# Optimization experiments

Hardware: AMD Instinct MI355X
Metric: run time of the kernel (lower is better)

## Reference

```python
import jax, jax.numpy as jnp
import numpy as np

HIDDEN = 768
NUM_BLOCKS = 8
BLOCK = HIDDEN // NUM_BLOCKS
BASE_THR, K_DECAY, MIN_THR = 0.01, 20.0, 0.0005


def _threshold(height, width):
    # wavenumber-dependent soft-shrink threshold T(k), shape [H, W//2+1]
    fu = jnp.fft.fftfreq(height, d=1.0).astype(jnp.float32)[:, None]
    fv = jnp.fft.rfftfreq(width, d=1.0).astype(jnp.float32)[None, :]
    k = jnp.sqrt(fu ** 2 + fv ** 2) * max(height, width)
    thr = BASE_THR * jnp.exp(-0.5 * (k / K_DECAY) ** 2)
    return jnp.maximum(thr, MIN_THR)


def setup_inputs() -> dict:
    key = jax.random.key(0)
    kx, k1, k2, k3, k4 = jax.random.split(key, 5)
    scale = 0.02
    x = jax.random.normal(kx, (4, 128, 128, HIDDEN), dtype=jnp.float32)
    w1 = scale * jax.random.normal(k1, (2, NUM_BLOCKS, BLOCK, BLOCK), dtype=jnp.float32)
    b1 = scale * jax.random.normal(k2, (2, NUM_BLOCKS, BLOCK), dtype=jnp.float32)
    w2 = scale * jax.random.normal(k3, (2, NUM_BLOCKS, BLOCK, BLOCK), dtype=jnp.float32)
    b2 = scale * jax.random.normal(k4, (2, NUM_BLOCKS, BLOCK), dtype=jnp.float32)
    return {"x": x, "w1": w1, "b1": b1, "w2": w2, "b2": b2}


def reference(x, w1, b1, w2, b2):
    dtype = x.dtype
    bias = x
    xf = x.astype(jnp.float32)
    B, H, W, C = xf.shape
    Wc = W // 2 + 1
    # rfft2 over spatial dims, orthonormal
    Xc = jnp.fft.rfft2(xf, axes=(1, 2), norm='ortho')
    Xc = Xc.reshape(B, H, Wc, NUM_BLOCKS, BLOCK)
    xr, xi = jnp.real(Xc), jnp.imag(Xc)
    mm = lambda t, w: jnp.einsum('bhwni,nio->bhwno', t, w)
    # complex block-diagonal 2-layer MLP
    o1r = jax.nn.relu(mm(xr, w1[0]) - mm(xi, w1[1]) + b1[0])
    o1i = jax.nn.relu(mm(xi, w1[0]) + mm(xr, w1[1]) + b1[1])
    o2r = mm(o1r, w2[0]) - mm(o1i, w2[1]) + b2[0]
    o2i = mm(o1i, w2[0]) + mm(o1r, w2[1]) + b2[1]
    # soft-shrink on complex magnitude with wavenumber-dependent threshold
    mag = jnp.sqrt(o2r ** 2 + o2i ** 2 + 1e-8)
    thr = _threshold(H, W)[None, :, :, None, None]  # [1,H,Wc,1,1]
    sf = jax.nn.relu(mag - thr) / mag
    Yc = (o2r * sf) + 1j * (o2i * sf)
    Yc = Yc.reshape(B, H, Wc, C)
    y = jnp.fft.irfft2(Yc, s=(H, W), axes=(1, 2), norm='ortho')
    return y.astype(dtype) + bias
```

## Files before the change

kernel.cpp:

```cpp
#include <hip/hip_runtime.h>
#include <hip/hip_bf16.h>
#include <math.h>


#define HD   768
#define NBLK 8
#define HH   128
#define WW   128
#define WC   65
#define NPOS (HH * WC)

constexpr float SC    = 0.08838834764831845f;
constexpr float TWOPI = 6.28318530717958647692f;

constexpr int TM_OFF     = 0;
constexpr int TW_OFF     = 49152;
constexpr int TWI_OFF    = 69632;
constexpr int WF_OFF     = 90112;
constexpr int WF_END_U16 = 679936;
constexpr size_t A_UINTS = (size_t)4 * NPOS * HD;

typedef __attribute__((ext_vector_type(8))) short short8;
typedef __attribute__((ext_vector_type(4))) float f32x4;

#define MFMA __builtin_amdgcn_mfma_f32_16x16x32_bf16

static __device__ inline unsigned short f2bf(float f) {
  __hip_bfloat16 h = __float2bfloat16(f);
  return __builtin_bit_cast(unsigned short, h);
}
static __device__ inline unsigned int pack2(float re, float im) {
  return (unsigned int)f2bf(re) | ((unsigned int)f2bf(im) << 16);
}
static __device__ inline float lo2f(unsigned int u) {
  return __builtin_bit_cast(float, u << 16);
}
static __device__ inline float hi2f(unsigned int u) {
  return __builtin_bit_cast(float, u & 0xffff0000u);
}

__global__ __launch_bounds__(256) void k_prep(const float* __restrict__ w1,
                                              const float* __restrict__ b1,
                                              const float* __restrict__ w2,
                                              const float* __restrict__ b2,
                                              unsigned short* __restrict__ wf,
                                              float* __restrict__ bpk) {
  const int blk = blockIdx.x, t = threadIdx.x;
  if (blk < 16) {
    const int layer = blk >> 3, n = blk & 7;
    const float* w  = layer ? w2 : w1;
    const float* bs = layer ? b2 : b1;
    unsigned short* dst = wf + WF_OFF + (size_t)blk * (72 * 512);
    for (int e = t; e < 72 * 512; e += 256) {
      int f = e >> 9, idx = e & 511;
      int kk = f / 12, nt = f - kk * 12;
      int lane = idx >> 3, j = idx & 7;
      int k  = kk * 32 + (lane >> 4) * 8 + j;
      int cc = nt * 16 + (lane & 15);
      float v;
      if (k < 96) v = (cc < 96) ? w[(size_t)n * 9216 + k * 96 + cc]
                                : w[(size_t)(8 + n) * 9216 + k * 96 + (cc - 96)];
      else        v = (cc < 96) ? -w[(size_t)(8 + n) * 9216 + (k - 96) * 96 + cc]
                                :  w[(size_t)n * 9216 + (k - 96) * 96 + (cc - 96)];
      dst[e] = f2bf(v);
    }
    for (int c = t; c < 192; c += 256)
      bpk[blk * 192 + c] = (c < 96) ? bs[n * 96 + c] : bs[(8 + n) * 96 + (c - 96)];
  } else if (blk == 16) {
    for (int e = t; e < 96 * 512; e += 256) {
      int f = e >> 9, idx = e & 511;
      int part = f >> 5, rem = f & 31, kot = rem >> 2, kk = rem & 3;
      int lane = idx >> 3, j = idx & 7;
      int ko = kot * 16 + (lane & 15);
      int r  = kk * 32 + (lane >> 4) * 8 + j;
      float sn, cs; sincosf((TWOPI / 128.f) * (float)((ko * r) & 127), &sn, &cs);
      float v = (part == 0) ? cs : (part == 1) ? sn : -sn;
      wf[TM_OFF + (size_t)f * 512 + idx] = f2bf(v * SC);
    }
  } else if (blk == 17) {
    for (int e = t; e < 40 * 512; e += 256) {
      int f = e >> 9, idx = e & 511;
      int mt = f >> 2, kk = f & 3;
      int lane = idx >> 3, j = idx & 7;
      int row = mt * 16 + (lane & 15);
      int r   = kk * 32 + (lane >> 4) * 8 + j;
      int kor = (row < 80) ? row : row - 80;
      float sn, cs; sincosf((TWOPI / 128.f) * (float)((kor * r) & 127), &sn, &cs);
      wf[TW_OFF + (size_t)f * 512 + idx] = f2bf((row < 80 ? cs : -sn) * SC);
    }
  } else {
    for (int e = t; e < 40 * 512; e += 256) {
      int f = e >> 9, idx = e & 511;
      int mt = f / 5, kk = f - mt * 5;
      int lane = idx >> 3, j = idx & 7;
      int wr = mt * 16 + (lane & 15);
      int k  = kk * 32 + (lane >> 4) * 8 + j;
      float v = 0.f;
      if (k < 80) {
        int kb = k;
        if (kb <= 64) {
          float sn, cs; sincosf((TWOPI / 128.f) * (float)((wr * kb) & 127), &sn, &cs);
          v = SC * ((kb == 0 || kb == 64) ? 1.f : 2.f) * cs;
        }
      } else {
        int kb = k - 80;
        if (kb >= 1 && kb <= 63) {
          float sn, cs; sincosf((TWOPI / 128.f) * (float)((wr * kb) & 127), &sn, &cs);
          v = -2.f * SC * sn;
        }
      }
      wf[TWI_OFF + (size_t)f * 512 + idx] = f2bf(v);
    }
  }
}

__global__ __launch_bounds__(256) void k_fft_w(const float* __restrict__ x,
                                               unsigned int* __restrict__ A,
                                               const unsigned short* __restrict__ wf) {
  __shared__ unsigned short Xt[64 * 136];
  const int h = blockIdx.x, c0 = blockIdx.y * 64, b = blockIdx.z, t = threadIdx.x;
  const int wv = t >> 6, lane = t & 63, l15 = lane & 15, lg = lane >> 4;
  const float* xp = x + ((size_t)(b * HH + h)) * WW * HD + c0;
  for (int idx = t; idx < 128 * 64; idx += 256) {
    int r = idx >> 6, ch = idx & 63;
    Xt[ch * 136 + r] = f2bf(xp[(size_t)r * HD + ch]);
  }
  __syncthreads();
  const unsigned short* tw = wf + TW_OFF;
  f32x4 acc[10];
#pragma unroll
  for (int m = 0; m < 10; ++m) acc[m] = { 0.f, 0.f, 0.f, 0.f };
#pragma unroll
  for (int kk = 0; kk < 4; ++kk) {
    short8 bq = *(const short8*)&Xt[(wv * 16 + l15) * 136 + kk * 32 + lg * 8];
#pragma unroll
    for (int m = 0; m < 10; ++m) {
      short8 a = *(const short8*)&tw[(size_t)(m * 4 + kk) * 512 + lane * 8];
      acc[m] = MFMA(a, bq, acc[m], 0, 0, 0);
    }
  }
  unsigned int* Ao = A + ((size_t)b * NPOS + h * WC) * HD + c0 + wv * 16 + l15;
#pragma unroll
  for (int q = 0; q < 5; ++q)
#pragma unroll
    for (int r = 0; r < 4; ++r) {
      int ko = q * 16 + lg * 4 + r;
      if (ko <= 64) Ao[(size_t)ko * HD] = pack2(acc[q][r], acc[5 + q][r]);
    }
}

__global__ __launch_bounds__(256) void k_ifft_w(const unsigned int* __restrict__ A,
                                                const unsigned int* __restrict__ Bp,
                                                float* __restrict__ out,
                                                const unsigned short* __restrict__ wf) {
  __shared__ unsigned short Zt[64 * 168];
  const int h = blockIdx.x, c0 = blockIdx.y * 64, b = blockIdx.z, t = threadIdx.x;
  const int wv = t >> 6, lane = t & 63, l15 = lane & 15, lg = lane >> 4;
  const size_t base = ((size_t)b * NPOS + h * WC) * HD + c0;
  for (int idx = t; idx < 65 * 64; idx += 256) {
    int kb = idx >> 6, ch = idx & 63;
    unsigned int uA = A[base + (size_t)kb * HD + ch];
    unsigned int uB = Bp[base + (size_t)kb * HD + ch];
    float re = lo2f(uA) + lo2f(uB);
    float im = hi2f(uA) + hi2f(uB);
    Zt[ch * 168 + kb]      = f2bf(re);
    Zt[ch * 168 + 80 + kb] = (kb == 0 || kb == 64) ? (unsigned short)0 : f2bf(im);
  }
  for (int idx = t; idx < 64 * 32; idx += 256) {
    int ch = idx >> 5, q = idx & 31;
    if (q < 30) {
      int kb = 65 + (q % 15), half = q / 15;
      Zt[ch * 168 + half * 80 + kb] = 0;
    }
  }
  __syncthreads();
  const unsigned short* twi = wf + TWI_OFF;
  f32x4 acc[8];
#pragma unroll
  for (int m = 0; m < 8; ++m) acc[m] = { 0.f, 0.f, 0.f, 0.f };
#pragma unroll
  for (int kk = 0; kk < 5; ++kk) {
    short8 bq = *(const short8*)&Zt[(wv * 16 + l15) * 168 + kk * 32 + lg * 8];
#pragma unroll
    for (int m = 0; m < 8; ++m) {
      short8 a = *(const short8*)&twi[(size_t)(m * 5 + kk) * 512 + lane * 8];
      acc[m] = MFMA(a, bq, acc[m], 0, 0, 0);
    }
  }
#pragma unroll
  for (int m = 0; m < 8; ++m)
#pragma unroll
    for (int r = 0; r < 4; ++r) {
      int wr = m * 16 + lg * 4 + r;
      size_t go = (((size_t)(b * HH + h)) * WW + wr) * HD + c0 + wv * 16 + l15;
      out[go] = acc[m][r];
    }
}

template <int FWD>
static __device__ inline void dft_gemm16(const unsigned short* Rb, const unsigned short* Ib,
                                         const unsigned short* tm, int rt, int cb, int lane,
                                         f32x4* aR, f32x4* aI) {
  const int l15 = lane & 15, lg = lane >> 4;
#pragma unroll
  for (int kkr = 0; kkr < 4; ++kkr) {
    const int r0 = kkr * 32 + lg * 8;
    short8 Ac = *(const short8*)&tm[(size_t)(0 * 32 + rt * 4 + kkr) * 512 + lane * 8];
    short8 As = *(const short8*)&tm[(size_t)(1 * 32 + rt * 4 + kkr) * 512 + lane * 8];
    short8 An = *(const short8*)&tm[(size_t)(2 * 32 + rt * 4 + kkr) * 512 + lane * 8];
#pragma unroll
    for (int c = 0; c < 3; ++c) {
      short8 zr = *(const short8*)&Rb[((cb + c) * 16 + l15) * 136 + r0];
      short8 zi = *(const short8*)&Ib[((cb + c) * 16 + l15) * 136 + r0];
      aR[c] = MFMA(Ac, zr, aR[c], 0, 0, 0);
      if constexpr (FWD) {
        aR[c] = MFMA(As, zi, aR[c], 0, 0, 0);
        aI[c] = MFMA(Ac, zi, aI[c], 0, 0, 0);
        aI[c] = MFMA(An, zr, aI[c], 0, 0, 0);
      } else {
        aR[c] = MFMA(An, zi, aR[c], 0, 0, 0);
        aI[c] = MFMA(Ac, zi, aI[c], 0, 0, 0);
        aI[c] = MFMA(As, zr, aI[c], 0, 0, 0);
      }
    }
  }
}

__global__ __launch_bounds__(1024) void k_mid(const unsigned int* __restrict__ A,
                                              unsigned int* __restrict__ Bp,
                                              const unsigned short* __restrict__ wf,
                                              const float* __restrict__ bpk) {
  __shared__ unsigned short Rb[13312], Ib[13312];
  __shared__ unsigned short WfL[12 * 512 / 1];
  const int kv = blockIdx.x, n = blockIdx.y, b = blockIdx.z, t = threadIdx.x;
  const int w = t >> 6, lane = t & 63, l15 = lane & 15, lg = lane >> 4;
  const int rt = w >> 1, cb = (w & 1) * 3;
  const size_t pbase = ((size_t)b * NPOS + kv) * HD + n * 96;
  const unsigned short* tm = wf + TM_OFF;
  const unsigned short* wf1 = wf + WF_OFF + (size_t)n * (72 * 512);
  const unsigned short* wf2 = wf + WF_OFF + (size_t)(8 + n) * (72 * 512);

#define LOAD_FRAGS(SRC, KP) \
  if (t < 768) ((int4*)WfL)[t] = ((const int4*)((SRC) + (KP) * 12 * 512))[t];

  for (int idx = t; idx < 128 * 96; idx += 1024) {
    int r = idx / 96, ch = idx - r * 96;
    unsigned int u = A[pbase + (size_t)r * (WC * HD) + ch];
    Rb[ch * 136 + r] = (unsigned short)(u & 0xffffu);
    Ib[ch * 136 + r] = (unsigned short)(u >> 16);
  }
  LOAD_FRAGS(wf1, 0);
  __syncthreads();

  f32x4 aR[3], aI[3];
#pragma unroll
  for (int c = 0; c < 3; ++c) { aR[c] = {0.f,0.f,0.f,0.f}; aI[c] = {0.f,0.f,0.f,0.f}; }
  dft_gemm16<1>(Rb, Ib, tm, rt, cb, lane, aR, aI);
  __syncthreads();

#pragma unroll
  for (int c = 0; c < 3; ++c)
#pragma unroll
    for (int r = 0; r < 4; ++r) {
      int row = rt * 16 + lg * 4 + r, ch = (cb + c) * 16 + l15;
      Rb[row * 104 + ch] = f2bf(aR[c][r]);
      Ib[row * 104 + ch] = f2bf(aI[c][r]);
    }
  __syncthreads();

  const int row_a = (rt * 16 + l15) * 104;
  f32x4 acc[6];
#pragma unroll
  for (int i = 0; i < 3; ++i) {
    float bv = bpk[n * 192 + (cb + i) * 16 + l15];
    acc[i] = { bv, bv, bv, bv };
    bv = bpk[n * 192 + (cb + i + 6) * 16 + l15];
    acc[3 + i] = { bv, bv, bv, bv };
  }

#define MLP_PAIR(k0)                                                             \
  {                                                                              \
    short8 aRf = *(const short8*)&Rb[row_a + (k0) * 32 + lg * 8];                \
    short8 aIf = *(const short8*)&Ib[row_a + (k0) * 32 + lg * 8];                \
    _Pragma("unroll")                                                            \
    for (int i = 0; i < 6; ++i) {                                                \
      int nt = cb + (i < 3 ? i : i + 3);                                         \
      short8 b0 = *(const short8*)&WfL[nt * 512 + lane * 8];                     \
      acc[i] = MFMA(aRf, b0, acc[i], 0, 0, 0);                                   \
      int nt2 = (nt < 6) ? nt + 6 : nt - 6;                                      \
      int4 nb = *(const int4*)&WfL[nt2 * 512 + lane * 8];                        \
      if (nt < 6) { nb.x ^= 0x80008000; nb.y ^= 0x80008000;                      \
                    nb.z ^= 0x80008000; nb.w ^= 0x80008000; }                    \
      acc[i] = MFMA(aIf, __builtin_bit_cast(short8, nb), acc[i], 0, 0, 0);       \
    }                                                                            \
  }

  MLP_PAIR(0);
  __syncthreads();
  LOAD_FRAGS(wf1, 1);
  __syncthreads();
  MLP_PAIR(1);
  __syncthreads();
  LOAD_FRAGS(wf1, 2);
  __syncthreads();
  MLP_PAIR(2);
  __syncthreads();

#pragma unroll
  for (int i = 0; i < 3; ++i)
#pragma unroll
    for (int r = 0; r < 4; ++r) {
      int row = rt * 16 + lg * 4 + r, ch = (cb + i) * 16 + l15;
      Rb[row * 104 + ch] = f2bf(fmaxf(acc[i][r], 0.f));
      Ib[row * 104 + ch] = f2bf(fmaxf(acc[3 + i][r], 0.f));
    }
  LOAD_FRAGS(wf2, 0);
  __syncthreads();

#pragma unroll
  for (int i = 0; i < 3; ++i) {
    float bv = bpk[(8 + n) * 192 + (cb + i) * 16 + l15];
    acc[i] = { bv, bv, bv, bv };
    bv = bpk[(8 + n) * 192 + (cb + i + 6) * 16 + l15];
    acc[3 + i] = { bv, bv, bv, bv };
  }
  MLP_PAIR(0);
  __syncthreads();
  LOAD_FRAGS(wf2, 1);
  __syncthreads();
  MLP_PAIR(1);
  __syncthreads();
  LOAD_FRAGS(wf2, 2);
  __syncthreads();
  MLP_PAIR(2);
  __syncthreads();

#pragma unroll
  for (int r = 0; r < 4; ++r) {
    int ko = rt * 16 + lg * 4 + r;
    float kus = (ko >= 64) ? (float)(ko - 128) : (float)ko;
    float k2v = kus * kus + (float)(kv * kv);
    float thr = fmaxf(0.01f * expf(-0.00125f * k2v), 0.0005f);
#pragma unroll
    for (int i = 0; i < 3; ++i) {
      float mr = acc[i][r], mi = acc[3 + i][r];
      float mag = sqrtf(mr * mr + mi * mi + 1e-8f);
      float sf = fmaxf(mag - thr, 0.f) / mag;
      int ch = (cb + i) * 16 + l15;
      Rb[ch * 136 + ko] = f2bf(mr * sf);
      Ib[ch * 136 + ko] = f2bf(mi * sf);
    }
  }
  __syncthreads();

#pragma unroll
  for (int c = 0; c < 3; ++c) { aR[c] = {0.f,0.f,0.f,0.f}; aI[c] = {0.f,0.f,0.f,0.f}; }
  dft_gemm16<0>(Rb, Ib, tm, rt, cb, lane, aR, aI);
#pragma unroll
  for (int c = 0; c < 3; ++c)
#pragma unroll
    for (int r = 0; r < 4; ++r) {
      int rr = rt * 16 + lg * 4 + r, ch = (cb + c) * 16 + l15;
      Bp[pbase + (size_t)rr * (WC * HD) + ch] = pack2(aR[c][r], aI[c][r]);
    }
#undef MLP_PAIR
#undef LOAD_FRAGS
}

extern "C" void kernel_launch(void* const* d_in, const int* in_sizes, int n_in,
                              void* d_out, int out_size, void* d_ws, size_t ws_size,
                              hipStream_t stream) {
  const float* x  = (const float*)d_in[0];
  const float* w1 = (const float*)d_in[1];
  const float* b1 = (const float*)d_in[2];
  const float* w2 = (const float*)d_in[3];
  const float* b2 = (const float*)d_in[4];
  float* out = (float*)d_out;
  unsigned int* A  = (unsigned int*)d_ws;
  unsigned int* Bp = A + A_UINTS;

  unsigned short* wf = (unsigned short*)(Bp + A_UINTS);
  float* bpk = (float*)(wf + WF_END_U16);

  k_prep<<<19, 256, 0, stream>>>(w1, b1, w2, b2, wf, bpk);
  k_fft_w<<<dim3(HH, HD / 64, 4), 256, 0, stream>>>(x, A, wf);
  k_mid<<<dim3(WC, NBLK, 4), 1024, 0, stream>>>(A, Bp, wf, bpk);
  k_ifft_w<<<dim3(HH, HD / 64, 4), 256, 0, stream>>>(A, Bp, out, wf);
}
```

Measured before the change: 411.8 us.

## Split fused mid kernel into separate H-FFT, MLP and inverse H-FFT kernels

The single 1024-thread kernel is replaced by three kernels. A forward FFT along H writes into Bp, a per-position block-diagonal MLP with soft-shrink runs in place on 64-position tiles, and an inverse FFT along H works in place on Bp. The goal is better occupancy and lower LDS pressure per block, plus MLP tiles that no longer depend on the FFT column layout. In exchange the complex spectrum makes two extra round trips through global memory.

```diff
diff --git a/kernel.cpp b/kernel.cpp
--- a/kernel.cpp
+++ b/kernel.cpp
@@ -198,74 +198,87 @@
 }
 
 template <int FWD>
-static __device__ inline void dft_gemm16(const unsigned short* Rb, const unsigned short* Ib,
-                                         const unsigned short* tm, int rt, int cb, int lane,
-                                         f32x4* aR, f32x4* aI) {
-  const int l15 = lane & 15, lg = lane >> 4;
+__global__ __launch_bounds__(256) void k_ffth(const unsigned int* __restrict__ SRC,
+                                              unsigned int* __restrict__ DST,
+                                              const unsigned short* __restrict__ wf) {
+  __shared__ unsigned short Rb[32 * 136], Ib[32 * 136];
+  const int kv = blockIdx.x, c0 = blockIdx.y * 32, b = blockIdx.z, t = threadIdx.x;
+  const int w = t >> 6, lane = t & 63, l15 = lane & 15, lg = lane >> 4;
+  const size_t base = (size_t)b * NPOS * HD;
+  for (int idx = t; idx < 128 * 32; idx += 256) {
+    int r = idx >> 5, ch = idx & 31;
+    unsigned int u = SRC[base + ((size_t)r * WC + kv) * HD + c0 + ch];
+    Rb[ch * 136 + r] = (unsigned short)(u & 0xffffu);
+    Ib[ch * 136 + r] = (unsigned short)(u >> 16);
+  }
+  __syncthreads();
+  const unsigned short* tm = wf + TM_OFF;
+  f32x4 accR[2][2], accI[2][2];
+#pragma unroll
+  for (int a = 0; a < 2; ++a)
+#pragma unroll
+    for (int c = 0; c < 2; ++c) { accR[a][c] = {0.f,0.f,0.f,0.f}; accI[a][c] = {0.f,0.f,0.f,0.f}; }
 #pragma unroll
   for (int kkr = 0; kkr < 4; ++kkr) {
     const int r0 = kkr * 32 + lg * 8;
-    short8 Ac = *(const short8*)&tm[(size_t)(0 * 32 + rt * 4 + kkr) * 512 + lane * 8];
-    short8 As = *(const short8*)&tm[(size_t)(1 * 32 + rt * 4 + kkr) * 512 + lane * 8];
-    short8 An = *(const short8*)&tm[(size_t)(2 * 32 + rt * 4 + kkr) * 512 + lane * 8];
-#pragma unroll
-    for (int c = 0; c < 3; ++c) {
-      short8 zr = *(const short8*)&Rb[((cb + c) * 16 + l15) * 136 + r0];
-      short8 zi = *(const short8*)&Ib[((cb + c) * 16 + l15) * 136 + r0];
-      aR[c] = MFMA(Ac, zr, aR[c], 0, 0, 0);
-      if constexpr (FWD) {
-        aR[c] = MFMA(As, zi, aR[c], 0, 0, 0);
-        aI[c] = MFMA(Ac, zi, aI[c], 0, 0, 0);
-        aI[c] = MFMA(An, zr, aI[c], 0, 0, 0);
-      } else {
-        aR[c] = MFMA(An, zi, aR[c], 0, 0, 0);
-        aI[c] = MFMA(Ac, zi, aI[c], 0, 0, 0);
-        aI[c] = MFMA(As, zr, aI[c], 0, 0, 0);
+#pragma unroll
+    for (int kot2 = 0; kot2 < 2; ++kot2) {
+      const int kot = w * 2 + kot2;
+      short8 Ac = *(const short8*)&tm[(size_t)(0 * 32 + kot * 4 + kkr) * 512 + lane * 8];
+      short8 As = *(const short8*)&tm[(size_t)(1 * 32 + kot * 4 + kkr) * 512 + lane * 8];
+      short8 An = *(const short8*)&tm[(size_t)(2 * 32 + kot * 4 + kkr) * 512 + lane * 8];
+#pragma unroll
+      for (int cht = 0; cht < 2; ++cht) {
+        short8 zr = *(const short8*)&Rb[(cht * 16 + l15) * 136 + r0];
+        short8 zi = *(const short8*)&Ib[(cht * 16 + l15) * 136 + r0];
+        accR[kot2][cht] = MFMA(Ac, zr, accR[kot2][cht], 0, 0, 0);
+        if constexpr (FWD) {
+          accR[kot2][cht] = MFMA(As, zi, accR[kot2][cht], 0, 0, 0);
+          accI[kot2][cht] = MFMA(Ac, zi, accI[kot2][cht], 0, 0, 0);
+          accI[kot2][cht] = MFMA(An, zr, accI[kot2][cht], 0, 0, 0);
+        } else {
+          accR[kot2][cht] = MFMA(An, zi, accR[kot2][cht], 0, 0, 0);
+          accI[kot2][cht] = MFMA(Ac, zi, accI[kot2][cht], 0, 0, 0);
+          accI[kot2][cht] = MFMA(As, zr, accI[kot2][cht], 0, 0, 0);
+        }
       }
     }
   }
-}
-
-__global__ __launch_bounds__(1024) void k_mid(const unsigned int* __restrict__ A,
-                                              unsigned int* __restrict__ Bp,
+#pragma unroll
+  for (int kot2 = 0; kot2 < 2; ++kot2)
+#pragma unroll
+    for (int cht = 0; cht < 2; ++cht)
+#pragma unroll
+      for (int r = 0; r < 4; ++r) {
+        int ko = (w * 2 + kot2) * 16 + lg * 4 + r;
+        DST[base + ((size_t)ko * WC + kv) * HD + c0 + cht * 16 + l15] =
+            pack2(accR[kot2][cht][r], accI[kot2][cht][r]);
+      }
+}
+
+__global__ __launch_bounds__(512) void k_mlp3(unsigned int* __restrict__ P,
                                               const unsigned short* __restrict__ wf,
                                               const float* __restrict__ bpk) {
-  __shared__ unsigned short Rb[13312], Ib[13312];
-  __shared__ unsigned short WfL[12 * 512 / 1];
-  const int kv = blockIdx.x, n = blockIdx.y, b = blockIdx.z, t = threadIdx.x;
+  __shared__ unsigned short Rq[64 * 104], Iq[64 * 104];
+  __shared__ unsigned short WfL[12 * 512];
+  const int p0 = blockIdx.x * 64, n = blockIdx.y, b = blockIdx.z, t = threadIdx.x;
   const int w = t >> 6, lane = t & 63, l15 = lane & 15, lg = lane >> 4;
   const int rt = w >> 1, cb = (w & 1) * 3;
-  const size_t pbase = ((size_t)b * NPOS + kv) * HD + n * 96;
-  const unsigned short* tm = wf + TM_OFF;
+  const size_t gbase = ((size_t)b * NPOS + p0) * HD + n * 96;
   const unsigned short* wf1 = wf + WF_OFF + (size_t)n * (72 * 512);
   const unsigned short* wf2 = wf + WF_OFF + (size_t)(8 + n) * (72 * 512);
 
-#define LOAD_FRAGS(SRC, KP) \
-  if (t < 768) ((int4*)WfL)[t] = ((const int4*)((SRC) + (KP) * 12 * 512))[t];
-
-  for (int idx = t; idx < 128 * 96; idx += 1024) {
-    int r = idx / 96, ch = idx - r * 96;
-    unsigned int u = A[pbase + (size_t)r * (WC * HD) + ch];
-    Rb[ch * 136 + r] = (unsigned short)(u & 0xffffu);
-    Ib[ch * 136 + r] = (unsigned short)(u >> 16);
+#define LOAD_FRAGS(SRC, KP)                                                       \
+  for (int idx = t; idx < 768; idx += 512)                                        \
+    ((int4*)WfL)[idx] = ((const int4*)((SRC) + (KP) * 12 * 512))[idx];
+
+  for (int idx = t; idx < 64 * 96; idx += 512) {
+    int pos = idx / 96, ch = idx - pos * 96;
+    unsigned int u = P[gbase + (size_t)pos * HD + ch];
+    Rq[pos * 104 + ch] = (unsigned short)(u & 0xffffu);
+    Iq[pos * 104 + ch] = (unsigned short)(u >> 16);
   }
   LOAD_FRAGS(wf1, 0);
-  __syncthreads();
-
-  f32x4 aR[3], aI[3];
-#pragma unroll
-  for (int c = 0; c < 3; ++c) { aR[c] = {0.f,0.f,0.f,0.f}; aI[c] = {0.f,0.f,0.f,0.f}; }
-  dft_gemm16<1>(Rb, Ib, tm, rt, cb, lane, aR, aI);
-  __syncthreads();
-
-#pragma unroll
-  for (int c = 0; c < 3; ++c)
-#pragma unroll
-    for (int r = 0; r < 4; ++r) {
-      int row = rt * 16 + lg * 4 + r, ch = (cb + c) * 16 + l15;
-      Rb[row * 104 + ch] = f2bf(aR[c][r]);
-      Ib[row * 104 + ch] = f2bf(aI[c][r]);
-    }
   __syncthreads();
 
   const int row_a = (rt * 16 + l15) * 104;
@@ -280,8 +293,8 @@
 
 #define MLP_PAIR(k0)                                                             \
   {                                                                              \
-    short8 aRf = *(const short8*)&Rb[row_a + (k0) * 32 + lg * 8];                \
-    short8 aIf = *(const short8*)&Ib[row_a + (k0) * 32 + lg * 8];                \
+    short8 aRf = *(const short8*)&Rq[row_a + (k0) * 32 + lg * 8];                \
+    short8 aIf = *(const short8*)&Iq[row_a + (k0) * 32 + lg * 8];                \
     _Pragma("unroll")                                                            \
     for (int i = 0; i < 6; ++i) {                                                \
       int nt = cb + (i < 3 ? i : i + 3);                                         \
@@ -311,8 +324,8 @@
 #pragma unroll
     for (int r = 0; r < 4; ++r) {
       int row = rt * 16 + lg * 4 + r, ch = (cb + i) * 16 + l15;
-      Rb[row * 104 + ch] = f2bf(fmaxf(acc[i][r], 0.f));
-      Ib[row * 104 + ch] = f2bf(fmaxf(acc[3 + i][r], 0.f));
+      Rq[row * 104 + ch] = f2bf(fmaxf(acc[i][r], 0.f));
+      Iq[row * 104 + ch] = f2bf(fmaxf(acc[3 + i][r], 0.f));
     }
   LOAD_FRAGS(wf2, 0);
   __syncthreads();
@@ -333,36 +346,23 @@
   LOAD_FRAGS(wf2, 2);
   __syncthreads();
   MLP_PAIR(2);
-  __syncthreads();
 
 #pragma unroll
   for (int r = 0; r < 4; ++r) {
-    int ko = rt * 16 + lg * 4 + r;
-    float kus = (ko >= 64) ? (float)(ko - 128) : (float)ko;
-    float k2v = kus * kus + (float)(kv * kv);
+    int pl = p0 + rt * 16 + lg * 4 + r;
+    int ku = pl / WC, kvv = pl - ku * WC;
+    float kus = (ku >= 64) ? (float)(ku - 128) : (float)ku;
+    float k2v = kus * kus + (float)(kvv * kvv);
     float thr = fmaxf(0.01f * expf(-0.00125f * k2v), 0.0005f);
 #pragma unroll
     for (int i = 0; i < 3; ++i) {
       float mr = acc[i][r], mi = acc[3 + i][r];
       float mag = sqrtf(mr * mr + mi * mi + 1e-8f);
       float sf = fmaxf(mag - thr, 0.f) / mag;
-      int ch = (cb + i) * 16 + l15;
-      Rb[ch * 136 + ko] = f2bf(mr * sf);
-      Ib[ch * 136 + ko] = f2bf(mi * sf);
-    }
-  }
-  __syncthreads();
-
-#pragma unroll
-  for (int c = 0; c < 3; ++c) { aR[c] = {0.f,0.f,0.f,0.f}; aI[c] = {0.f,0.f,0.f,0.f}; }
-  dft_gemm16<0>(Rb, Ib, tm, rt, cb, lane, aR, aI);
-#pragma unroll
-  for (int c = 0; c < 3; ++c)
-#pragma unroll
-    for (int r = 0; r < 4; ++r) {
-      int rr = rt * 16 + lg * 4 + r, ch = (cb + c) * 16 + l15;
-      Bp[pbase + (size_t)rr * (WC * HD) + ch] = pack2(aR[c][r], aI[c][r]);
-    }
+      P[gbase + (size_t)(rt * 16 + lg * 4 + r) * HD + (cb + i) * 16 + l15] =
+          pack2(mr * sf, mi * sf);
+    }
+  }
 #undef MLP_PAIR
 #undef LOAD_FRAGS
 }
@@ -384,6 +384,8 @@
 
   k_prep<<<19, 256, 0, stream>>>(w1, b1, w2, b2, wf, bpk);
   k_fft_w<<<dim3(HH, HD / 64, 4), 256, 0, stream>>>(x, A, wf);
-  k_mid<<<dim3(WC, NBLK, 4), 1024, 0, stream>>>(A, Bp, wf, bpk);
+  k_ffth<1><<<dim3(WC, HD / 32, 4), 256, 0, stream>>>(A, Bp, wf);
+  k_mlp3<<<dim3(NPOS / 64, NBLK, 4), 512, 0, stream>>>(Bp, wf, bpk);
+  k_ffth<0><<<dim3(WC, HD / 32, 4), 256, 0, stream>>>(Bp, Bp, wf);
   k_ifft_w<<<dim3(HH, HD / 64, 4), 256, 0, stream>>>(A, Bp, out, wf);
 }
```

Result: slower. 456.8 us (+10.9%).
